# Kernel tuning notes

Measured on AMD Instinct MI355X. Metric: run time of the kernel, lower is better.

## Reference

```python
import jax, jax.numpy as jnp
import numpy as np

HID = 16

def _lrconv(x, edge_index, edge_attr, w1, b1, w2, b2):
    # flow='target_to_source': x_i = x[edge_index[0]], x_j = x[edge_index[1]],
    # aggregate (max) at edge_index[0].
    src = edge_index[0]
    dst = edge_index[1]
    m = jnp.concatenate([x[src], x[dst], edge_attr], axis=-1)  # [E, 2*in+edge]
    m = jax.nn.relu(m @ w1 + b1)
    m = jax.nn.relu(m @ w2 + b2)  # [E, out], all >= 0
    agg = jax.ops.segment_max(m, src, num_segments=x.shape[0])
    # empty segments get -inf in jax; PyG fills with 0. Messages are ReLU'd (>=0),
    # so clamping at 0 is exact.
    return jnp.maximum(agg, 0.0)

def _glorot(key, shape):
    fan_in, fan_out = shape
    lim = float(np.sqrt(6.0 / (fan_in + fan_out)))
    return jax.random.uniform(key, shape, jnp.float32, -lim, lim)

def setup_inputs() -> dict:
    key = jax.random.key(0)
    ks = jax.random.split(key, 16)
    N, E = 100000, 1600000
    x = jax.random.normal(ks[0], (N, 4), jnp.float32)
    edge_index = jax.random.randint(ks[1], (2, E), 0, N, jnp.int64)
    edge_attr = jax.random.normal(ks[2], (E, 8), jnp.float32)
    # conv1: in=4 -> cat dim 4*2+8=16
    c1_w1 = _glorot(ks[3], (16, HID)); c1_b1 = jnp.zeros((HID,), jnp.float32)
    c1_w2 = _glorot(ks[4], (HID, 16)); c1_b2 = jnp.zeros((16,), jnp.float32)
    # conv2: in=16 -> cat dim 16*2+8=40
    c2_w1 = _glorot(ks[5], (40, HID)); c2_b1 = jnp.zeros((HID,), jnp.float32)
    c2_w2 = _glorot(ks[6], (HID, 16)); c2_b2 = jnp.zeros((16,), jnp.float32)
    l1_w = _glorot(ks[7], (16, 16)); l1_b = jnp.zeros((16,), jnp.float32)
    l2_w = _glorot(ks[8], (16, 1)); l2_b = jnp.zeros((1,), jnp.float32)
    return {"x": x, "edge_index": edge_index, "edge_attr": edge_attr,
            "c1_w1": c1_w1, "c1_b1": c1_b1, "c1_w2": c1_w2, "c1_b2": c1_b2,
            "c2_w1": c2_w1, "c2_b1": c2_b1, "c2_w2": c2_w2, "c2_b2": c2_b2,
            "l1_w": l1_w, "l1_b": l1_b, "l2_w": l2_w, "l2_b": l2_b}

def reference(x, edge_index, edge_attr,
              c1_w1, c1_b1, c1_w2, c1_b2,
              c2_w1, c2_b1, c2_w2, c2_b2,
              l1_w, l1_b, l2_w, l2_b):
    h = _lrconv(x, edge_index, edge_attr, c1_w1, c1_b1, c1_w2, c1_b2)   # [N,16]
    h = _lrconv(h, edge_index, edge_attr, c2_w1, c2_b1, c2_w2, c2_b2)   # [N,16]
    h = jax.nn.relu(h @ l1_w + l1_b)
    return h @ l2_w + l2_b  # [N,1]
```

## Files before the change

kernel.cpp:

```cpp
#include <hip/hip_runtime.h>
#include <hip/hip_fp16.h>

#define CHUNK 1024

typedef _Float16 half8 __attribute__((ext_vector_type(8)));
typedef float floatx4 __attribute__((ext_vector_type(4)));

__device__ __forceinline__ unsigned int pack2(float a, float b) {
    __half2 h = __floats2half2_rn(a, b);
    return *(unsigned int*)&h;
}
__device__ __forceinline__ float2 unpack2(unsigned int u) {
    __half2 h = *(__half2*)&u;
    return __half22float2(h);
}

__global__ __launch_bounds__(256) void rank_cvt(
    const int* __restrict__ ei, const float* __restrict__ ea,
    int* __restrict__ deg, unsigned short* __restrict__ r,
    _Float16* __restrict__ eah, int E)
{
    int e = blockIdx.x * 256 + threadIdx.x;
    if (e >= E) return;
    r[e] = (unsigned short)atomicAdd(&deg[ei[e]], 1);
    float4 a0 = *(const float4*)(ea + (size_t)e * 8);
    float4 a1 = *(const float4*)(ea + (size_t)e * 8 + 4);
    half8 h;
    h[0] = (_Float16)a0.x; h[1] = (_Float16)a0.y;
    h[2] = (_Float16)a0.z; h[3] = (_Float16)a0.w;
    h[4] = (_Float16)a1.x; h[5] = (_Float16)a1.y;
    h[6] = (_Float16)a1.z; h[7] = (_Float16)a1.w;
    *(half8*)(eah + (size_t)e * 8) = h;
}

__global__ __launch_bounds__(256) void scan_chunk_sums(
    const int* __restrict__ v, int* __restrict__ csum, int N)
{
    __shared__ int s[256];
    int base = blockIdx.x * CHUNK;
    int t = threadIdx.x;
    int acc = 0;
    #pragma unroll
    for (int i = 0; i < CHUNK / 256; ++i) {
        int idx = base + t + i * 256;
        if (idx < N) acc += v[idx];
    }
    s[t] = acc; __syncthreads();
    for (int o = 128; o > 0; o >>= 1) {
        if (t < o) s[t] += s[t + o];
        __syncthreads();
    }
    if (t == 0) csum[blockIdx.x] = s[0];
}

__global__ void scan_chunk_off(
    const int* __restrict__ csum, int* __restrict__ coff, int nch)
{
    if (threadIdx.x == 0 && blockIdx.x == 0) {
        int acc = 0;
        for (int i = 0; i < nch; ++i) { coff[i] = acc; acc += csum[i]; }
    }
}

__global__ __launch_bounds__(256) void scan_within_excl(
    const int* __restrict__ deg, int* __restrict__ pos,
    const int* __restrict__ coff, int N)
{
    __shared__ int s[256];
    int t = threadIdx.x;
    int base = blockIdx.x * CHUNK + t * 4;
    int v0 = 0, v1 = 0, v2 = 0, v3 = 0;
    if (base + 0 < N) v0 = deg[base + 0];
    if (base + 1 < N) v1 = deg[base + 1];
    if (base + 2 < N) v2 = deg[base + 2];
    if (base + 3 < N) v3 = deg[base + 3];
    s[t] = v0 + v1 + v2 + v3;
    __syncthreads();
    for (int o = 1; o < 256; o <<= 1) {
        int add = (t >= o) ? s[t - o] : 0;
        __syncthreads();
        s[t] += add;
        __syncthreads();
    }
    int run = coff[blockIdx.x] + (t > 0 ? s[t - 1] : 0);
    if (base + 0 < N) pos[base + 0] = run; run += v0;
    if (base + 1 < N) pos[base + 1] = run; run += v1;
    if (base + 2 < N) pos[base + 2] = run; run += v2;
    if (base + 3 < N) pos[base + 3] = run;
}

__global__ __launch_bounds__(256) void edge_mlp1(
    const float* __restrict__ x,
    const int*   __restrict__ ei,
    const _Float16* __restrict__ eah,
    const int*   __restrict__ pos,
    const unsigned short* __restrict__ r,
    const float* __restrict__ w1, const float* __restrict__ b1,
    const float* __restrict__ w2, const float* __restrict__ b2,
    _Float16* __restrict__ m2h,
    int E)
{
    __shared__ _Float16 itm[4][4][16][24];
    int tid = threadIdx.x;
    int w = tid >> 6, lane = tid & 63;
    int e16 = lane & 15, q = lane >> 4;
    int ntiles = (E + 63) >> 6;
    int tile = blockIdx.x * 4 + w;
    if (tile >= ntiles) return;
    int ebase = tile << 6;
    int e = ebase + lane;

    int s_l = 0, d_l = 0, p_l = 0;
    if (e < E) {
        s_l = ei[e];
        d_l = ei[E + e];
        p_l = pos[s_l] + (int)r[e];
    }

    half8 B1, B2;
    #pragma unroll
    for (int j = 0; j < 8; ++j) { B1[j] = (_Float16)0.f; B2[j] = (_Float16)0.f; }
    if (q < 2) {
        #pragma unroll
        for (int j = 0; j < 8; ++j) {
            B1[j] = (_Float16)w1[(8 * q + j) * 16 + e16];
            B2[j] = (_Float16)w2[(8 * q + j) * 16 + e16];
        }
    }
    float b1c = b1[e16], b2c = b2[e16];

    half8 A[4];
    #pragma unroll
    for (int t = 0; t < 4; ++t) {
        int st = __shfl(s_l, 16 * t + e16, 64);
        int dt = __shfl(d_l, 16 * t + e16, 64);
        half8 a;
        #pragma unroll
        for (int j = 0; j < 8; ++j) a[j] = (_Float16)0.f;
        int et = ebase + 16 * t + e16;
        if (q == 0 && et < E) {
            float4 xs = *(const float4*)(x + (size_t)st * 4);
            float4 xd = *(const float4*)(x + (size_t)dt * 4);
            a[0] = (_Float16)xs.x; a[1] = (_Float16)xs.y;
            a[2] = (_Float16)xs.z; a[3] = (_Float16)xs.w;
            a[4] = (_Float16)xd.x; a[5] = (_Float16)xd.y;
            a[6] = (_Float16)xd.z; a[7] = (_Float16)xd.w;
        } else if (q == 1 && et < E) {
            a = *(const half8*)(eah + (size_t)et * 8);
        }
        A[t] = a;
    }

    floatx4 C[4];
    #pragma unroll
    for (int t = 0; t < 4; ++t) {
        floatx4 c = {b1c, b1c, b1c, b1c};
        C[t] = __builtin_amdgcn_mfma_f32_16x16x32_f16(A[t], B1, c, 0, 0, 0);
    }
    #pragma unroll
    for (int t = 0; t < 4; ++t)
        #pragma unroll
        for (int i = 0; i < 4; ++i)
            itm[w][t][4 * q + i][e16] = (_Float16)fmaxf(C[t][i], 0.0f);
    __builtin_amdgcn_wave_barrier();

    half8 A2[4];
    #pragma unroll
    for (int t = 0; t < 4; ++t) {
        half8 a;
        #pragma unroll
        for (int j = 0; j < 8; ++j) a[j] = (_Float16)0.f;
        if (q < 2) a = *(const half8*)&itm[w][t][e16][8 * q];
        A2[t] = a;
    }
    __builtin_amdgcn_wave_barrier();
    floatx4 C2[4];
    #pragma unroll
    for (int t = 0; t < 4; ++t) {
        floatx4 c = {b2c, b2c, b2c, b2c};
        C2[t] = __builtin_amdgcn_mfma_f32_16x16x32_f16(A2[t], B2, c, 0, 0, 0);
    }
    #pragma unroll
    for (int t = 0; t < 4; ++t)
        #pragma unroll
        for (int i = 0; i < 4; ++i)
            itm[w][t][4 * q + i][e16] = (_Float16)C2[t][i];
    __builtin_amdgcn_wave_barrier();

    if (e < E) {
        half8 lo = *(const half8*)&itm[w][q][e16][0];
        half8 hi = *(const half8*)&itm[w][q][e16][8];
        *(half8*)(m2h + (size_t)p_l * 16)     = lo;
        *(half8*)(m2h + (size_t)p_l * 16 + 8) = hi;
    }
}

__global__ __launch_bounds__(256) void edge_mlp2(
    const float* __restrict__ hw_s,
    const unsigned short* __restrict__ hw_dh,
    const int*   __restrict__ ei,
    const _Float16* __restrict__ eah,
    const int*   __restrict__ pos,
    const unsigned short* __restrict__ r,
    const float* __restrict__ w1,
    const float* __restrict__ w2, const float* __restrict__ b2,
    _Float16* __restrict__ m2h, int E)
{
    __shared__ _Float16 itm[4][4][16][24];
    int tid = threadIdx.x;
    int w = tid >> 6, lane = tid & 63;
    int e16 = lane & 15, q = lane >> 4;
    const __half* hwd = (const __half*)hw_dh;
    int ntiles = (E + 63) >> 6;
    int tile = blockIdx.x * 4 + w;
    if (tile >= ntiles) return;
    int ebase = tile << 6;
    int e = ebase + lane;

    int s_l = 0, d_l = 0, p_l = 0;
    if (e < E) {
        s_l = ei[e];
        d_l = ei[E + e];
        p_l = pos[s_l] + (int)r[e];
    }

    half8 B1, B2;
    #pragma unroll
    for (int j = 0; j < 8; ++j) { B1[j] = (_Float16)0.f; B2[j] = (_Float16)0.f; }
    if (q == 0) {
        #pragma unroll
        for (int j = 0; j < 8; ++j)
            B1[j] = (_Float16)w1[(32 + j) * 16 + e16];
    }
    if (q < 2) {
        #pragma unroll
        for (int j = 0; j < 8; ++j)
            B2[j] = (_Float16)w2[(8 * q + j) * 16 + e16];
    }
    float b2c = b2[e16];

    half8 A[4];
    #pragma unroll
    for (int t = 0; t < 4; ++t) {
        half8 a;
        #pragma unroll
        for (int j = 0; j < 8; ++j) a[j] = (_Float16)0.f;
        int et = ebase + 16 * t + e16;
        if (q == 0 && et < E)
            a = *(const half8*)(eah + (size_t)et * 8);
        A[t] = a;
    }

    floatx4 C[4];
    #pragma unroll
    for (int t = 0; t < 4; ++t) {
        floatx4 c;
        #pragma unroll
        for (int i = 0; i < 4; ++i) {
            int li = 16 * t + 4 * q + i;
            int s = __shfl(s_l, li, 64);
            int d = __shfl(d_l, li, 64);
            int rr = ebase + li;
            float v = 0.0f;
            if (rr < E) {
                v = hw_s[(size_t)s * 16 + e16]
                  + __half2float(hwd[(size_t)d * 16 + e16]);
            }
            c[i] = v;
        }
        C[t] = __builtin_amdgcn_mfma_f32_16x16x32_f16(A[t], B1, c, 0, 0, 0);
    }
    #pragma unroll
    for (int t = 0; t < 4; ++t)
        #pragma unroll
        for (int i = 0; i < 4; ++i)
            itm[w][t][4 * q + i][e16] = (_Float16)fmaxf(C[t][i], 0.0f);
    __builtin_amdgcn_wave_barrier();

    half8 A2[4];
    #pragma unroll
    for (int t = 0; t < 4; ++t) {
        half8 a;
        #pragma unroll
        for (int j = 0; j < 8; ++j) a[j] = (_Float16)0.f;
        if (q < 2) a = *(const half8*)&itm[w][t][e16][8 * q];
        A2[t] = a;
    }
    __builtin_amdgcn_wave_barrier();
    floatx4 C2[4];
    #pragma unroll
    for (int t = 0; t < 4; ++t) {
        floatx4 c = {b2c, b2c, b2c, b2c};
        C2[t] = __builtin_amdgcn_mfma_f32_16x16x32_f16(A2[t], B2, c, 0, 0, 0);
    }
    #pragma unroll
    for (int t = 0; t < 4; ++t)
        #pragma unroll
        for (int i = 0; i < 4; ++i)
            itm[w][t][4 * q + i][e16] = (_Float16)C2[t][i];
    __builtin_amdgcn_wave_barrier();

    if (e < E) {
        half8 lo = *(const half8*)&itm[w][q][e16][0];
        half8 hi = *(const half8*)&itm[w][q][e16][8];
        *(half8*)(m2h + (size_t)p_l * 16)     = lo;
        *(half8*)(m2h + (size_t)p_l * 16 + 8) = hi;
    }
}

__global__ __launch_bounds__(256) void segmax1_hw(
    const _Float16* __restrict__ m2h, const int* __restrict__ pos,
    const float* __restrict__ cw1, const float* __restrict__ cb1,
    float* __restrict__ hw_s, unsigned short* __restrict__ hw_dh,
    int N, int E)
{
    int tid = threadIdx.x;
    int n = blockIdx.x * 32 + (tid >> 3);
    if (n >= N) return;
    int g = tid & 7;
    int start = pos[n];
    int end = (n + 1 < N) ? pos[n + 1] : E;

    float acc[16];
    #pragma unroll
    for (int j = 0; j < 16; ++j) acc[j] = 0.0f;

    for (int k = start + g; k < end; k += 8) {
        uint4 u0 = *(const uint4*)(m2h + (size_t)k * 16);
        uint4 u1 = *(const uint4*)(m2h + (size_t)k * 16 + 8);
        float2 f;
        f = unpack2(u0.x); acc[0]  = fmaxf(acc[0],  f.x); acc[1]  = fmaxf(acc[1],  f.y);
        f = unpack2(u0.y); acc[2]  = fmaxf(acc[2],  f.x); acc[3]  = fmaxf(acc[3],  f.y);
        f = unpack2(u0.z); acc[4]  = fmaxf(acc[4],  f.x); acc[5]  = fmaxf(acc[5],  f.y);
        f = unpack2(u0.w); acc[6]  = fmaxf(acc[6],  f.x); acc[7]  = fmaxf(acc[7],  f.y);
        f = unpack2(u1.x); acc[8]  = fmaxf(acc[8],  f.x); acc[9]  = fmaxf(acc[9],  f.y);
        f = unpack2(u1.y); acc[10] = fmaxf(acc[10], f.x); acc[11] = fmaxf(acc[11], f.y);
        f = unpack2(u1.z); acc[12] = fmaxf(acc[12], f.x); acc[13] = fmaxf(acc[13], f.y);
        f = unpack2(u1.w); acc[14] = fmaxf(acc[14], f.x); acc[15] = fmaxf(acc[15], f.y);
    }
    #pragma unroll
    for (int mask = 1; mask < 8; mask <<= 1) {
        #pragma unroll
        for (int j = 0; j < 16; ++j)
            acc[j] = fmaxf(acc[j], __shfl_xor(acc[j], mask, 64));
    }

    int j0 = 2 * g, j1 = 2 * g + 1;
    float hs0 = cb1[j0], hs1 = cb1[j1], hd0 = 0.0f, hd1 = 0.0f;
    #pragma unroll
    for (int k = 0; k < 16; ++k) {
        float ak = acc[k];
        hs0 = fmaf(ak, cw1[k * 16 + j0], hs0);
        hs1 = fmaf(ak, cw1[k * 16 + j1], hs1);
        hd0 = fmaf(ak, cw1[(16 + k) * 16 + j0], hd0);
        hd1 = fmaf(ak, cw1[(16 + k) * 16 + j1], hd1);
    }
    *(float2*)(hw_s + (size_t)n * 16 + j0) = make_float2(hs0, hs1);
    ((unsigned int*)hw_dh)[(size_t)n * 8 + g] = pack2(hd0, hd1);
}

__global__ __launch_bounds__(256) void segmax2_head(
    const _Float16* __restrict__ m2h, const int* __restrict__ pos,
    const float* __restrict__ l1w, const float* __restrict__ l1b,
    const float* __restrict__ l2w, const float* __restrict__ l2b,
    float* __restrict__ out, int N, int E)
{
    int tid = threadIdx.x;
    int n = blockIdx.x * 32 + (tid >> 3);
    if (n >= N) return;
    int g = tid & 7;
    int start = pos[n];
    int end = (n + 1 < N) ? pos[n + 1] : E;

    float acc[16];
    #pragma unroll
    for (int j = 0; j < 16; ++j) acc[j] = 0.0f;

    for (int k = start + g; k < end; k += 8) {
        uint4 u0 = *(const uint4*)(m2h + (size_t)k * 16);
        uint4 u1 = *(const uint4*)(m2h + (size_t)k * 16 + 8);
        float2 f;
        f = unpack2(u0.x); acc[0]  = fmaxf(acc[0],  f.x); acc[1]  = fmaxf(acc[1],  f.y);
        f = unpack2(u0.y); acc[2]  = fmaxf(acc[2],  f.x); acc[3]  = fmaxf(acc[3],  f.y);
        f = unpack2(u0.z); acc[4]  = fmaxf(acc[4],  f.x); acc[5]  = fmaxf(acc[5],  f.y);
        f = unpack2(u0.w); acc[6]  = fmaxf(acc[6],  f.x); acc[7]  = fmaxf(acc[7],  f.y);
        f = unpack2(u1.x); acc[8]  = fmaxf(acc[8],  f.x); acc[9]  = fmaxf(acc[9],  f.y);
        f = unpack2(u1.y); acc[10] = fmaxf(acc[10], f.x); acc[11] = fmaxf(acc[11], f.y);
        f = unpack2(u1.z); acc[12] = fmaxf(acc[12], f.x); acc[13] = fmaxf(acc[13], f.y);
        f = unpack2(u1.w); acc[14] = fmaxf(acc[14], f.x); acc[15] = fmaxf(acc[15], f.y);
    }
    #pragma unroll
    for (int mask = 1; mask < 8; mask <<= 1) {
        #pragma unroll
        for (int j = 0; j < 16; ++j)
            acc[j] = fmaxf(acc[j], __shfl_xor(acc[j], mask, 64));
    }

    float t2[16];
    #pragma unroll
    for (int j = 0; j < 16; ++j) t2[j] = l1b[j];
    #pragma unroll
    for (int kk = 0; kk < 16; ++kk) {
        float ak = acc[kk];
        #pragma unroll
        for (int j = 0; j < 16; ++j) t2[j] = fmaf(ak, l1w[kk * 16 + j], t2[j]);
    }
    float r2 = l2b[0];
    #pragma unroll
    for (int j = 0; j < 16; ++j) r2 = fmaf(fmaxf(t2[j], 0.0f), l2w[j], r2);
    if (g == 0) out[n] = r2;
}

extern "C" void kernel_launch(void* const* d_in, const int* in_sizes, int n_in,
                              void* d_out, int out_size, void* d_ws, size_t ws_size,
                              hipStream_t stream)
{
    const float* x     = (const float*)d_in[0];
    const int*   ei    = (const int*)  d_in[1];
    const float* ea    = (const float*)d_in[2];
    const float* c1_w1 = (const float*)d_in[3];
    const float* c1_b1 = (const float*)d_in[4];
    const float* c1_w2 = (const float*)d_in[5];
    const float* c1_b2 = (const float*)d_in[6];
    const float* c2_w1 = (const float*)d_in[7];
    const float* c2_b1 = (const float*)d_in[8];
    const float* c2_w2 = (const float*)d_in[9];
    const float* c2_b2 = (const float*)d_in[10];
    const float* l1_w  = (const float*)d_in[11];
    const float* l1_b  = (const float*)d_in[12];
    const float* l2_w  = (const float*)d_in[13];
    const float* l2_b  = (const float*)d_in[14];
    float* out = (float*)d_out;

    const int N = in_sizes[0] / 4;
    const int E = in_sizes[2] / 8;
    const int nch = (N + CHUNK - 1) / CHUNK;

    const int BLK = 256;
    const int egrid = (E + BLK - 1) / BLK;
    const int ggrid = (N + 31) / 32;
    const int ntiles64 = (E + 63) >> 6;
    const int mgrid = (ntiles64 + 3) / 4;

    size_t szN16f = (size_t)N * 16 * 4;
    size_t szN16h = (size_t)N * 16 * 2;
    size_t szN    = ((size_t)N * 4 + 15) & ~(size_t)15;
    size_t szEh   = ((size_t)E * 2 + 15) & ~(size_t)15;
    size_t szE16  = (size_t)E * 16;

    size_t pos_off  = 0;
    size_t r_off    = pos_off  + szN;
    size_t hws_off  = r_off    + szEh;
    size_t hwdh_off = hws_off  + szN16f;
    size_t eah_off  = hwdh_off + szN16h;
    size_t m2h_off  = eah_off  + szE16;
    size_t deg_off  = m2h_off;
    size_t cs_off   = deg_off  + szN;
    size_t cf_off   = cs_off   + 4096;

    int*            pos  = (int*)  ((char*)d_ws + pos_off);
    unsigned short* r    = (unsigned short*)((char*)d_ws + r_off);
    float*          hw_s = (float*)((char*)d_ws + hws_off);
    unsigned short* hwdh = (unsigned short*)((char*)d_ws + hwdh_off);
    _Float16*       eah  = (_Float16*)((char*)d_ws + eah_off);
    _Float16*       m2h  = (_Float16*)((char*)d_ws + m2h_off);
    int*            deg  = (int*)  ((char*)d_ws + deg_off);
    int*            csum = (int*)  ((char*)d_ws + cs_off);
    int*            coff = (int*)  ((char*)d_ws + cf_off);

    hipMemsetAsync(deg, 0, (size_t)N * 4, stream);
    rank_cvt<<<egrid, BLK, 0, stream>>>(ei, ea, deg, r, eah, E);
    scan_chunk_sums<<<nch, BLK, 0, stream>>>(deg, csum, N);
    scan_chunk_off<<<1, 64, 0, stream>>>(csum, coff, nch);
    scan_within_excl<<<nch, BLK, 0, stream>>>(deg, pos, coff, N);
    edge_mlp1<<<mgrid, BLK, 0, stream>>>(x, ei, eah, pos, r,
                                         c1_w1, c1_b1, c1_w2, c1_b2, m2h, E);
    segmax1_hw<<<ggrid, BLK, 0, stream>>>(m2h, pos, c2_w1, c2_b1,
                                          hw_s, hwdh, N, E);
    edge_mlp2<<<mgrid, BLK, 0, stream>>>(hw_s, hwdh, ei, eah, pos, r,
                                         c2_w1, c2_w2, c2_b2, m2h, E);
    segmax2_head<<<ggrid, BLK, 0, stream>>>(m2h, pos, l1_w, l1_b, l2_w, l2_b,
                                            out, N, E);
}
```

Before: 363.1 us.

## Spread degree-count atomics over per-node sub-buckets and parallelize chunk-offset scan

The degree counting atomics are split into 16 sub-buckets per node, picked from the edge's block index, so contention on each node counter drops. The CSR offsets now come from scanning the N*16 bucket array, and the edge kernels read the bucket base while the segment kernels read each node's first bucket. The single-thread chunk-offset scan becomes a 256-thread block scan, because the chunk count grows sixteenfold. The trade-off is a 16x larger count/offset array: more memset, scan traffic and scattered pos reads, with little collision benefit given about 16 edges per node.

```diff
diff --git a/kernel.cpp b/kernel.cpp
--- a/kernel.cpp
+++ b/kernel.cpp
@@ -2,6 +2,7 @@
 #include <hip/hip_fp16.h>
 
 #define CHUNK 1024
+#define NBKT 16
 
 typedef _Float16 half8 __attribute__((ext_vector_type(8)));
 typedef float floatx4 __attribute__((ext_vector_type(4)));
@@ -22,7 +23,8 @@
 {
     int e = blockIdx.x * 256 + threadIdx.x;
     if (e >= E) return;
-    r[e] = (unsigned short)atomicAdd(&deg[ei[e]], 1);
+    int bkt = (e >> 8) & (NBKT - 1);
+    r[e] = (unsigned short)atomicAdd(&deg[(size_t)ei[e] * NBKT + bkt], 1);
     float4 a0 = *(const float4*)(ea + (size_t)e * 8);
     float4 a1 = *(const float4*)(ea + (size_t)e * 8 + 4);
     half8 h;
@@ -53,12 +55,28 @@
     if (t == 0) csum[blockIdx.x] = s[0];
 }
 
-__global__ void scan_chunk_off(
+__global__ __launch_bounds__(256) void scan_chunk_off(
     const int* __restrict__ csum, int* __restrict__ coff, int nch)
 {
-    if (threadIdx.x == 0 && blockIdx.x == 0) {
-        int acc = 0;
-        for (int i = 0; i < nch; ++i) { coff[i] = acc; acc += csum[i]; }
+    __shared__ int s[256];
+    __shared__ int carry;
+    int t = threadIdx.x;
+    if (t == 0) carry = 0;
+    __syncthreads();
+    for (int base = 0; base < nch; base += 256) {
+        int v = (base + t < nch) ? csum[base + t] : 0;
+        s[t] = v; __syncthreads();
+        for (int o = 1; o < 256; o <<= 1) {
+            int add = (t >= o) ? s[t - o] : 0;
+            __syncthreads();
+            s[t] += add;
+            __syncthreads();
+        }
+        int excl = carry + (t > 0 ? s[t - 1] : 0);
+        if (base + t < nch) coff[base + t] = excl;
+        __syncthreads();
+        if (t == 0) carry += s[255];
+        __syncthreads();
     }
 }
 
@@ -114,7 +132,7 @@
     if (e < E) {
         s_l = ei[e];
         d_l = ei[E + e];
-        p_l = pos[s_l] + (int)r[e];
+        p_l = pos[(size_t)s_l * NBKT + ((e >> 8) & (NBKT - 1))] + (int)r[e];
     }
 
     half8 B1, B2;
@@ -221,7 +239,7 @@
     if (e < E) {
         s_l = ei[e];
         d_l = ei[E + e];
-        p_l = pos[s_l] + (int)r[e];
+        p_l = pos[(size_t)s_l * NBKT + ((e >> 8) & (NBKT - 1))] + (int)r[e];
     }
 
     half8 B1, B2;
@@ -318,8 +336,8 @@
     int n = blockIdx.x * 32 + (tid >> 3);
     if (n >= N) return;
     int g = tid & 7;
-    int start = pos[n];
-    int end = (n + 1 < N) ? pos[n + 1] : E;
+    int start = pos[(size_t)n * NBKT];
+    int end = (n + 1 < N) ? pos[(size_t)(n + 1) * NBKT] : E;
 
     float acc[16];
     #pragma unroll
@@ -369,8 +387,8 @@
     int n = blockIdx.x * 32 + (tid >> 3);
     if (n >= N) return;
     int g = tid & 7;
-    int start = pos[n];
-    int end = (n + 1 < N) ? pos[n + 1] : E;
+    int start = pos[(size_t)n * NBKT];
+    int end = (n + 1 < N) ? pos[(size_t)(n + 1) * NBKT] : E;
 
     float acc[16];
     #pragma unroll
@@ -434,7 +452,8 @@
 
     const int N = in_sizes[0] / 4;
     const int E = in_sizes[2] / 8;
-    const int nch = (N + CHUNK - 1) / CHUNK;
+    const int M = N * NBKT;
+    const int nch = (M + CHUNK - 1) / CHUNK;
 
     const int BLK = 256;
     const int egrid = (E + BLK - 1) / BLK;
@@ -444,19 +463,19 @@
 
     size_t szN16f = (size_t)N * 16 * 4;
     size_t szN16h = (size_t)N * 16 * 2;
-    size_t szN    = ((size_t)N * 4 + 15) & ~(size_t)15;
+    size_t szPos  = ((size_t)M * 4 + 15) & ~(size_t)15;
     size_t szEh   = ((size_t)E * 2 + 15) & ~(size_t)15;
     size_t szE16  = (size_t)E * 16;
 
     size_t pos_off  = 0;
-    size_t r_off    = pos_off  + szN;
+    size_t r_off    = pos_off  + szPos;
     size_t hws_off  = r_off    + szEh;
     size_t hwdh_off = hws_off  + szN16f;
     size_t eah_off  = hwdh_off + szN16h;
     size_t m2h_off  = eah_off  + szE16;
     size_t deg_off  = m2h_off;
-    size_t cs_off   = deg_off  + szN;
-    size_t cf_off   = cs_off   + 4096;
+    size_t cs_off   = deg_off  + szPos;
+    size_t cf_off   = cs_off   + 16384;
 
     int*            pos  = (int*)  ((char*)d_ws + pos_off);
     unsigned short* r    = (unsigned short*)((char*)d_ws + r_off);
@@ -468,11 +487,11 @@
     int*            csum = (int*)  ((char*)d_ws + cs_off);
     int*            coff = (int*)  ((char*)d_ws + cf_off);
 
-    hipMemsetAsync(deg, 0, (size_t)N * 4, stream);
+    hipMemsetAsync(deg, 0, (size_t)M * 4, stream);
     rank_cvt<<<egrid, BLK, 0, stream>>>(ei, ea, deg, r, eah, E);
-    scan_chunk_sums<<<nch, BLK, 0, stream>>>(deg, csum, N);
-    scan_chunk_off<<<1, 64, 0, stream>>>(csum, coff, nch);
-    scan_within_excl<<<nch, BLK, 0, stream>>>(deg, pos, coff, N);
+    scan_chunk_sums<<<nch, BLK, 0, stream>>>(deg, csum, M);
+    scan_chunk_off<<<1, 256, 0, stream>>>(csum, coff, nch);
+    scan_within_excl<<<nch, BLK, 0, stream>>>(deg, pos, coff, M);
     edge_mlp1<<<mgrid, BLK, 0, stream>>>(x, ei, eah, pos, r,
                                          c1_w1, c1_b1, c1_w2, c1_b2, m2h, E);
     segmax1_hw<<<ggrid, BLK, 0, stream>>>(m2h, pos, c2_w1, c2_b1,
```

Result: slower. 382.9 us (+5.4%).
